# Performance work log

Measured on AMD Instinct MI355X. Metric: run time of the kernel, lower is better.

Reference implementation:

```python
import jax, jax.numpy as jnp
import numpy as np

N = 50000   # num nodes
R = 8       # num relations
E = 800000  # num edges
IN, HID, OUT = 128, 128, 64


def rgcn_layer(x, src, dst, etype, W, root, bias):
    """PyG-style RGCNConv: per-relation mean aggregation + root weight + bias.
    x: [N, I], W: [R, I, O], root: [I, O], bias: [O]."""
    O = W.shape[-1]
    # transform node features once per relation: [R, N, O]
    xr = jnp.einsum('ni,rio->rno', x, W)
    # per-edge message = relation-specific transform of source node
    m = xr[etype, src]                      # [E, O] gather
    # mean-aggregate per (relation, dst) pair, then sum over relations
    idx = etype * N + dst                   # combined segment id in [0, R*N)
    s = jax.ops.segment_sum(m, idx, num_segments=R * N)          # [R*N, O]
    c = jax.ops.segment_sum(jnp.ones_like(etype, dtype=m.dtype), idx,
                            num_segments=R * N)                   # [R*N]
    agg = (s / jnp.maximum(c, 1.0)[:, None]).reshape(R, N, O).sum(axis=0)
    return agg + x @ root + bias


def setup_inputs() -> dict:
    key = jax.random.key(0)
    ks = jax.random.split(key, 16)
    x = jax.random.normal(ks[0], (N, IN), dtype=jnp.float32)
    edge_index = jax.random.randint(ks[1], (2, E), 0, N, dtype=jnp.int32)
    edge_type = jax.random.randint(ks[2], (E,), 0, R, dtype=jnp.int32)
    dims = [(IN, HID), (HID, HID), (HID, HID), (HID, OUT)]
    inp = {"x": x, "edge_index": edge_index, "edge_type": edge_type}
    for li, (i, o) in enumerate(dims):
        sc = 1.0 / np.sqrt(i)
        inp[f"W{li+1}"] = jax.random.normal(ks[3 + 3 * li], (R, i, o), dtype=jnp.float32) * sc
        inp[f"root{li+1}"] = jax.random.normal(ks[4 + 3 * li], (i, o), dtype=jnp.float32) * sc
        inp[f"b{li+1}"] = jnp.zeros((o,), dtype=jnp.float32)
    return inp


def reference(x, edge_index, edge_type,
              W1, root1, b1, W2, root2, b2,
              W3, root3, b3, W4, root4, b4):
    src, dst = edge_index[0], edge_index[1]
    h = jax.nn.relu(rgcn_layer(x, src, dst, edge_type, W1, root1, b1))
    h = jax.nn.relu(rgcn_layer(h, src, dst, edge_type, W2, root2, b2))
    h = jax.nn.relu(rgcn_layer(h, src, dst, edge_type, W3, root3, b3))
    h = rgcn_layer(h, src, dst, edge_type, W4, root4, b4)
    return jax.nn.log_softmax(h, axis=1)
```

## Files before the change

kernel.cpp:

```cpp
#include <hip/hip_runtime.h>
#include <math.h>

#define NN 50000
#define RR 8
#define EE 800000
#define RN 400000
#define DIN 128
#define K1 1024
#define KTOT 1152
#define NBLK 391
#define LDWH 648

#define OFF_HB0  0UL
#define OFF_HB1  12800000UL
#define OFF_XB   25600000UL
#define OFF_LG   38400000UL
#define OFF_WT   51200000UL
#define OFF_OFFS 52379648UL
#define OFF_CUR  53979776UL
#define OFF_SRT  55579776UL
#define OFF_BS   58779776UL
#define WS_NEED  58783872UL

typedef short bf16x8 __attribute__((ext_vector_type(8)));
typedef float f32x4 __attribute__((ext_vector_type(4)));

__device__ __forceinline__ unsigned f2bf(float f) {
    unsigned x = __float_as_uint(f);
    return (x + 0x7fffu + ((x >> 16) & 1u)) >> 16;
}
__device__ __forceinline__ float bflo(unsigned p) { return __uint_as_float(p << 16); }
__device__ __forceinline__ float bfhi(unsigned p) { return __uint_as_float(p & 0xffff0000u); }

__global__ void k_cvt(const float* __restrict__ x, ushort* __restrict__ xb) {
    int i = blockIdx.x * 256 + threadIdx.x;
    if (i >= NN * 32) return;
    float4 v = ((const float4*)x)[i];
    ushort4 o;
    o.x = (ushort)f2bf(v.x); o.y = (ushort)f2bf(v.y);
    o.z = (ushort)f2bf(v.z); o.w = (ushort)f2bf(v.w);
    ((ushort4*)xb)[i] = o;
}

__global__ void k_wtall(const float* __restrict__ W0, const float* __restrict__ R0,
                        const float* __restrict__ W1, const float* __restrict__ R1,
                        const float* __restrict__ W2, const float* __restrict__ R2,
                        const float* __restrict__ W3, const float* __restrict__ R3,
                        ushort* __restrict__ WT) {
    int b = blockIdx.x;
    int layer = (b < 384) ? (b >> 7) : 3;
    int o = (b < 384) ? (b & 127) : (b - 384);
    int O = (layer == 3) ? 64 : 128;
    const float* W  = (layer == 0) ? W0 : (layer == 1) ? W1 : (layer == 2) ? W2 : W3;
    const float* Rt = (layer == 0) ? R0 : (layer == 1) ? R1 : (layer == 2) ? R2 : R3;
    ushort* dst = WT + (size_t)layer * 147456;
    for (int k = threadIdx.x; k < KTOT; k += 256) {
        float v = (k < K1)
            ? W[(size_t)(k >> 7) * 128 * O + (size_t)(k & 127) * O + o]
            : Rt[(size_t)(k - K1) * O + o];
        dst[(size_t)o * KTOT + k] = (ushort)f2bf(v);
    }
}

__global__ void k_hist(const int* __restrict__ ei, const int* __restrict__ et,
                       int* __restrict__ hist) {
    int e = blockIdx.x * blockDim.x + threadIdx.x;
    if (e >= EE) return;
    atomicAdd(&hist[ei[EE + e] * RR + et[e]], 1);
}

__global__ void k_scan1(const int* __restrict__ hist, int* __restrict__ offs,
                        int* __restrict__ bsums) {
    __shared__ int tmp[1024];
    int tid = threadIdx.x;
    int g = blockIdx.x * 1024 + tid;
    int v = (g < RN) ? hist[g] : 0;
    tmp[tid] = v;
    __syncthreads();
    for (int off = 1; off < 1024; off <<= 1) {
        int t = tmp[tid];
        if (tid >= off) t += tmp[tid - off];
        __syncthreads();
        tmp[tid] = t;
        __syncthreads();
    }
    if (g < RN) offs[g] = tmp[tid] - v;
    if (tid == 1023) bsums[blockIdx.x] = tmp[1023];
}

__global__ void k_scan2(int* __restrict__ bsums) {
    __shared__ int tmp[1024];
    int tid = threadIdx.x;
    int v = (tid < NBLK) ? bsums[tid] : 0;
    tmp[tid] = v;
    __syncthreads();
    for (int off = 1; off < 1024; off <<= 1) {
        int t = tmp[tid];
        if (tid >= off) t += tmp[tid - off];
        __syncthreads();
        tmp[tid] = t;
        __syncthreads();
    }
    if (tid < NBLK) bsums[tid] = tmp[tid] - v;
}

__global__ void k_scan3(int* __restrict__ offs, const int* __restrict__ bsums) {
    int g = blockIdx.x * 1024 + threadIdx.x;
    if (g < RN) offs[g] += bsums[blockIdx.x];
    else if (g == RN) offs[RN] = EE;
}

__global__ void k_scatter(const int* __restrict__ ei, const int* __restrict__ et,
                          const int* __restrict__ offs, int* __restrict__ cur,
                          int* __restrict__ ssrc) {
    int e = blockIdx.x * blockDim.x + threadIdx.x;
    if (e >= EE) return;
    int s = ei[EE + e] * RR + et[e];
    ssrc[offs[s] + atomicAdd(&cur[s], 1)] = ei[e];
}

template<int O, bool RELU, bool SMAX>
__global__ __launch_bounds__(512) void k_fused(
        const ushort* __restrict__ hb, const int* __restrict__ offs,
        const int* __restrict__ ssrc, const ushort* __restrict__ WT,
        const float* __restrict__ bias, void* __restrict__ outv) {
    __shared__ ushort As[32 * LDWH];
    const int tid = threadIdx.x;
    const int lane = tid & 63;
    const int w = tid >> 6;
    const int q = lane >> 4;
    const int ll = lane & 15;
    const int nbase = blockIdx.x * 32;
    const uint4* h16 = (const uint4*)hb;

    constexpr int NTILE = O / 16;
    const int cw = w % NTILE;
    const int mt0 = (NTILE == 8) ? 0 : (w / NTILE);
    constexpr int NMT = (NTILE == 8) ? 2 : 1;
    const int lr = lane & 15, hi = lane >> 4;
    f32x4 acc[NMT] = {};

    for (int half = 0; half < 2; ++half) {
        const int rbase = half * 4;
        for (int i = 0; i < 2; ++i) {
            int nlA = w * 4 + i * 2;
            int nlB = nlA + 1;
            int nA = min(nbase + nlA, NN - 1);
            int nB = min(nbase + nlB, NN - 1);
            int b = offs[((lane < 32) ? nA : nB) * 8 + rbase + min(lane & 31, 4)];
            int b0A = __shfl(b, 0),  b4A = __shfl(b, 4);
            int b0B = __shfl(b, 32), b4B = __shfl(b, 36);
            int nbA = b4A - b0A, nbB = b4B - b0B;
            int svA = ssrc[min(b0A + min(lane, max(nbA - 1, 0)), EE - 1)];
            int svB = ssrc[min(b0B + min(lane, max(nbB - 1, 0)), EE - 1)];
            int begA = __shfl(b, q),      endA = __shfl(b, q + 1);
            int begB = __shfl(b, 32 + q), endB = __shfl(b, 32 + q + 1);
            int lenA = endA - begA, lenB = endB - begB;
            int mxA = max(max(__shfl(lenA, 0), __shfl(lenA, 16)),
                          max(__shfl(lenA, 32), __shfl(lenA, 48)));
            int mxB = max(max(__shfl(lenB, 0), __shfl(lenB, 16)),
                          max(__shfl(lenB, 32), __shfl(lenB, 48)));
            int mx = max(mxA, mxB);
            int beglA = begA - b0A, beglB = begB - b0B;
            float aA0 = 0.f, aA1 = 0.f, aA2 = 0.f, aA3 = 0.f;
            float aA4 = 0.f, aA5 = 0.f, aA6 = 0.f, aA7 = 0.f;
            float aB0 = 0.f, aB1 = 0.f, aB2 = 0.f, aB3 = 0.f;
            float aB4 = 0.f, aB5 = 0.f, aB6 = 0.f, aB7 = 0.f;
            for (int j = 0; j < mx; j += 4) {
                int eA = beglA + j, eB = beglB + j;
                int sA0 = __shfl(svA, min(eA, 63));
                int sA1 = __shfl(svA, min(eA + 1, 63));
                int sA2 = __shfl(svA, min(eA + 2, 63));
                int sA3 = __shfl(svA, min(eA + 3, 63));
                int sB0 = __shfl(svB, min(eB, 63));
                int sB1 = __shfl(svB, min(eB + 1, 63));
                int sB2 = __shfl(svB, min(eB + 2, 63));
                int sB3 = __shfl(svB, min(eB + 3, 63));
                if (eA + 3 >= 64) {
                    sA0 = ssrc[min(b0A + eA, EE - 1)];
                    sA1 = ssrc[min(b0A + eA + 1, EE - 1)];
                    sA2 = ssrc[min(b0A + eA + 2, EE - 1)];
                    sA3 = ssrc[min(b0A + eA + 3, EE - 1)];
                }
                if (eB + 3 >= 64) {
                    sB0 = ssrc[min(b0B + eB, EE - 1)];
                    sB1 = ssrc[min(b0B + eB + 1, EE - 1)];
                    sB2 = ssrc[min(b0B + eB + 2, EE - 1)];
                    sB3 = ssrc[min(b0B + eB + 3, EE - 1)];
                }
                uint4 uA0 = h16[(size_t)sA0 * 16 + ll];
                uint4 uA1 = h16[(size_t)sA1 * 16 + ll];
                uint4 uA2 = h16[(size_t)sA2 * 16 + ll];
                uint4 uA3 = h16[(size_t)sA3 * 16 + ll];
                uint4 uB0 = h16[(size_t)sB0 * 16 + ll];
                uint4 uB1 = h16[(size_t)sB1 * 16 + ll];
                uint4 uB2 = h16[(size_t)sB2 * 16 + ll];
                uint4 uB3 = h16[(size_t)sB3 * 16 + ll];
                if (j < lenA) {
                    aA0 += bflo(uA0.x); aA1 += bfhi(uA0.x);
                    aA2 += bflo(uA0.y); aA3 += bfhi(uA0.y);
                    aA4 += bflo(uA0.z); aA5 += bfhi(uA0.z);
                    aA6 += bflo(uA0.w); aA7 += bfhi(uA0.w);
                }
                if (j + 1 < lenA) {
                    aA0 += bflo(uA1.x); aA1 += bfhi(uA1.x);
                    aA2 += bflo(uA1.y); aA3 += bfhi(uA1.y);
                    aA4 += bflo(uA1.z); aA5 += bfhi(uA1.z);
                    aA6 += bflo(uA1.w); aA7 += bfhi(uA1.w);
                }
                if (j + 2 < lenA) {
                    aA0 += bflo(uA2.x); aA1 += bfhi(uA2.x);
                    aA2 += bflo(uA2.y); aA3 += bfhi(uA2.y);
                    aA4 += bflo(uA2.z); aA5 += bfhi(uA2.z);
                    aA6 += bflo(uA2.w); aA7 += bfhi(uA2.w);
                }
                if (j + 3 < lenA) {
                    aA0 += bflo(uA3.x); aA1 += bfhi(uA3.x);
                    aA2 += bflo(uA3.y); aA3 += bfhi(uA3.y);
                    aA4 += bflo(uA3.z); aA5 += bfhi(uA3.z);
                    aA6 += bflo(uA3.w); aA7 += bfhi(uA3.w);
                }
                if (j < lenB) {
                    aB0 += bflo(uB0.x); aB1 += bfhi(uB0.x);
                    aB2 += bflo(uB0.y); aB3 += bfhi(uB0.y);
                    aB4 += bflo(uB0.z); aB5 += bfhi(uB0.z);
                    aB6 += bflo(uB0.w); aB7 += bfhi(uB0.w);
                }
                if (j + 1 < lenB) {
                    aB0 += bflo(uB1.x); aB1 += bfhi(uB1.x);
                    aB2 += bflo(uB1.y); aB3 += bfhi(uB1.y);
                    aB4 += bflo(uB1.z); aB5 += bfhi(uB1.z);
                    aB6 += bflo(uB1.w); aB7 += bfhi(uB1.w);
                }
                if (j + 2 < lenB) {
                    aB0 += bflo(uB2.x); aB1 += bfhi(uB2.x);
                    aB2 += bflo(uB2.y); aB3 += bfhi(uB2.y);
                    aB4 += bflo(uB2.z); aB5 += bfhi(uB2.z);
                    aB6 += bflo(uB2.w); aB7 += bfhi(uB2.w);
                }
                if (j + 3 < lenB) {
                    aB0 += bflo(uB3.x); aB1 += bfhi(uB3.x);
                    aB2 += bflo(uB3.y); aB3 += bfhi(uB3.y);
                    aB4 += bflo(uB3.z); aB5 += bfhi(uB3.z);
                    aB6 += bflo(uB3.w); aB7 += bfhi(uB3.w);
                }
            }
            float invA = 1.0f / (float)max(lenA, 1);
            float invB = 1.0f / (float)max(lenB, 1);
            uint4 oA, oB;
            oA.x = f2bf(aA0 * invA) | (f2bf(aA1 * invA) << 16);
            oA.y = f2bf(aA2 * invA) | (f2bf(aA3 * invA) << 16);
            oA.z = f2bf(aA4 * invA) | (f2bf(aA5 * invA) << 16);
            oA.w = f2bf(aA6 * invA) | (f2bf(aA7 * invA) << 16);
            oB.x = f2bf(aB0 * invB) | (f2bf(aB1 * invB) << 16);
            oB.y = f2bf(aB2 * invB) | (f2bf(aB3 * invB) << 16);
            oB.z = f2bf(aB4 * invB) | (f2bf(aB5 * invB) << 16);
            oB.w = f2bf(aB6 * invB) | (f2bf(aB7 * invB) << 16);
            *(uint4*)(&As[nlA * LDWH + (q * 16 + ll) * 8]) = oA;
            *(uint4*)(&As[nlB * LDWH + (q * 16 + ll) * 8]) = oB;
        }
        if (half == 1) {
            int row = tid >> 4;
            int cc = tid & 15;
            uint4 v = h16[(size_t)min(nbase + row, NN - 1) * 16 + cc];
            *(uint4*)(&As[row * LDWH + (64 + cc) * 8]) = v;
        }
        __syncthreads();
        const int KS = (half == 0) ? 16 : 20;
        const ushort* wcol = WT + (size_t)(cw * 16 + lr) * KTOT
                                + half * 512 + hi * 8;
        for (int ks = 0; ks < KS; ++ks) {
            bf16x8 bb = *(const bf16x8*)(wcol + ks * 32);
            int g = ks * 4 + hi;
#pragma unroll
            for (int m = 0; m < NMT; ++m) {
                int row = (mt0 + m) * 16 + lr;
                bf16x8 a = *(const bf16x8*)(&As[row * LDWH + g * 8]);
                acc[m] = __builtin_amdgcn_mfma_f32_16x16x32_bf16(a, bb, acc[m], 0, 0, 0);
            }
        }
        __syncthreads();
    }
    int col = cw * 16 + lr;
    float bs = bias[col];
    if (!SMAX) {
#pragma unroll
        for (int m = 0; m < NMT; ++m) {
#pragma unroll
            for (int j = 0; j < 4; ++j) {
                int row = nbase + (mt0 + m) * 16 + hi * 4 + j;
                if (row >= NN) continue;
                float v = acc[m][j] + bs;
                if (RELU) v = fmaxf(v, 0.f);
                ((ushort*)outv)[(size_t)row * O + col] = (ushort)f2bf(v);
            }
        }
    } else {
        float* Asf = (float*)As;
#pragma unroll
        for (int j = 0; j < 4; ++j) {
            int rl = mt0 * 16 + hi * 4 + j;
            Asf[rl * 65 + col] = acc[0][j] + bs;
        }
        __syncthreads();
        for (int rr = 0; rr < 4; ++rr) {
            int rl = w * 4 + rr;
            float v = Asf[rl * 65 + lane];
            float m = v;
#pragma unroll
            for (int off = 32; off; off >>= 1) m = fmaxf(m, __shfl_xor(m, off, 64));
            float e = expf(v - m);
            float s = e;
#pragma unroll
            for (int off = 32; off; off >>= 1) s += __shfl_xor(s, off, 64);
            int row = nbase + rl;
            if (row < NN)
                ((float*)outv)[(size_t)row * 64 + lane] = v - m - logf(s);
        }
    }
}

extern "C" void kernel_launch(void* const* d_in, const int* in_sizes, int n_in,
                              void* d_out, int out_size, void* d_ws, size_t ws_size,
                              hipStream_t stream) {
    const float* x  = (const float*)d_in[0];
    const int*   ei = (const int*)d_in[1];
    const int*   et = (const int*)d_in[2];
    const float* W[4]    = {(const float*)d_in[3], (const float*)d_in[6],
                            (const float*)d_in[9], (const float*)d_in[12]};
    const float* root[4] = {(const float*)d_in[4], (const float*)d_in[7],
                            (const float*)d_in[10], (const float*)d_in[13]};
    const float* bias[4] = {(const float*)d_in[5], (const float*)d_in[8],
                            (const float*)d_in[11], (const float*)d_in[14]};

    if (ws_size < WS_NEED) return;

    char* ws = (char*)d_ws;
    ushort* hb0  = (ushort*)(ws + OFF_HB0);
    ushort* hb1  = (ushort*)(ws + OFF_HB1);
    ushort* xb   = (ushort*)(ws + OFF_XB);
    ushort* WT   = (ushort*)(ws + OFF_WT);
    int*   offs  = (int*)(ws + OFF_OFFS);
    int*   cur   = (int*)(ws + OFF_CUR);
    int*   ssrc  = (int*)(ws + OFF_SRT);
    int*   bsums = (int*)(ws + OFF_BS);
    ushort* WTl[4] = {WT, WT + 147456, WT + 2 * 147456, WT + 3 * 147456};

    k_cvt<<<(NN * 32 + 255) / 256, 256, 0, stream>>>(x, xb);
    k_wtall<<<448, 256, 0, stream>>>(W[0], root[0], W[1], root[1],
                                     W[2], root[2], W[3], root[3], WT);

    hipMemsetAsync(cur, 0, RN * sizeof(int), stream);
    k_hist<<<(EE + 255) / 256, 256, 0, stream>>>(ei, et, cur);
    k_scan1<<<NBLK, 1024, 0, stream>>>(cur, offs, bsums);
    k_scan2<<<1, 1024, 0, stream>>>(bsums);
    k_scan3<<<NBLK + 1, 1024, 0, stream>>>(offs, bsums);
    hipMemsetAsync(cur, 0, RN * sizeof(int), stream);
    k_scatter<<<(EE + 255) / 256, 256, 0, stream>>>(ei, et, offs, cur, ssrc);

    const int G = (NN + 31) / 32;
    k_fused<128, true,  false><<<G, 512, 0, stream>>>(xb,  offs, ssrc, WTl[0], bias[0], hb0);
    k_fused<128, true,  false><<<G, 512, 0, stream>>>(hb0, offs, ssrc, WTl[1], bias[1], hb1);
    k_fused<128, true,  false><<<G, 512, 0, stream>>>(hb1, offs, ssrc, WTl[2], bias[2], hb0);
    k_fused<64,  false, true ><<<G, 512, 0, stream>>>(hb0, offs, ssrc, WTl[3], bias[3], d_out);
}
```

Before: 515.8 us.

## Aggregate all eight relations before a single full-K MFMA pass

The fused gather+GEMM kernel used to run two halves, each aggregating four relations into shared memory and then running a partial MFMA pass. It now aggregates all eight relations first, writing one row of 1152 bf16 values per node into a larger shared tile, and then runs one fully unrolled 36-step MFMA loop. The aim is to cut barrier count and loop overhead and to load the neighbour-offset row and edge list once per node pair instead of once per half. In exchange the shared tile roughly doubles (about 74KB), which may reduce how many blocks fit per CU, and the edge gather and GEMM phases no longer interleave across halves.

```diff
diff --git a/kernel.cpp b/kernel.cpp
--- a/kernel.cpp
+++ b/kernel.cpp
@@ -9,12 +9,11 @@
 #define K1 1024
 #define KTOT 1152
 #define NBLK 391
-#define LDWH 648
+#define LDW 1160
 
 #define OFF_HB0  0UL
 #define OFF_HB1  12800000UL
 #define OFF_XB   25600000UL
-#define OFF_LG   38400000UL
 #define OFF_WT   51200000UL
 #define OFF_OFFS 52379648UL
 #define OFF_CUR  53979776UL
@@ -124,7 +123,7 @@
         const ushort* __restrict__ hb, const int* __restrict__ offs,
         const int* __restrict__ ssrc, const ushort* __restrict__ WT,
         const float* __restrict__ bias, void* __restrict__ outv) {
-    __shared__ ushort As[32 * LDWH];
+    __shared__ ushort As[32 * LDW];
     const int tid = threadIdx.x;
     const int lane = tid & 63;
     const int w = tid >> 6;
@@ -133,28 +132,22 @@
     const int nbase = blockIdx.x * 32;
     const uint4* h16 = (const uint4*)hb;
 
-    constexpr int NTILE = O / 16;
-    const int cw = w % NTILE;
-    const int mt0 = (NTILE == 8) ? 0 : (w / NTILE);
-    constexpr int NMT = (NTILE == 8) ? 2 : 1;
-    const int lr = lane & 15, hi = lane >> 4;
-    f32x4 acc[NMT] = {};
-
-    for (int half = 0; half < 2; ++half) {
-        const int rbase = half * 4;
-        for (int i = 0; i < 2; ++i) {
-            int nlA = w * 4 + i * 2;
-            int nlB = nlA + 1;
-            int nA = min(nbase + nlA, NN - 1);
-            int nB = min(nbase + nlB, NN - 1);
-            int b = offs[((lane < 32) ? nA : nB) * 8 + rbase + min(lane & 31, 4)];
-            int b0A = __shfl(b, 0),  b4A = __shfl(b, 4);
-            int b0B = __shfl(b, 32), b4B = __shfl(b, 36);
-            int nbA = b4A - b0A, nbB = b4B - b0B;
-            int svA = ssrc[min(b0A + min(lane, max(nbA - 1, 0)), EE - 1)];
-            int svB = ssrc[min(b0B + min(lane, max(nbB - 1, 0)), EE - 1)];
-            int begA = __shfl(b, q),      endA = __shfl(b, q + 1);
-            int begB = __shfl(b, 32 + q), endB = __shfl(b, 32 + q + 1);
+    for (int i = 0; i < 2; ++i) {
+        int nlA = w * 4 + i * 2;
+        int nlB = nlA + 1;
+        int nA = min(nbase + nlA, NN - 1);
+        int nB = min(nbase + nlB, NN - 1);
+        int b = offs[((lane < 32) ? nA : nB) * 8 + min(lane & 31, 8)];
+        int b0A = __shfl(b, 0),  b8A = __shfl(b, 8);
+        int b0B = __shfl(b, 32), b8B = __shfl(b, 40);
+        int nbA = b8A - b0A, nbB = b8B - b0B;
+        int svA = ssrc[min(b0A + min(lane, max(nbA - 1, 0)), EE - 1)];
+        int svB = ssrc[min(b0B + min(lane, max(nbB - 1, 0)), EE - 1)];
+#pragma unroll
+        for (int p = 0; p < 2; ++p) {
+            int r = p * 4 + q;
+            int begA = __shfl(b, r),      endA = __shfl(b, r + 1);
+            int begB = __shfl(b, 32 + r), endB = __shfl(b, 32 + r + 1);
             int lenA = endA - begA, lenB = endB - begB;
             int mxA = max(max(__shfl(lenA, 0), __shfl(lenA, 16)),
                           max(__shfl(lenA, 32), __shfl(lenA, 48)));
@@ -256,30 +249,34 @@
             oB.y = f2bf(aB2 * invB) | (f2bf(aB3 * invB) << 16);
             oB.z = f2bf(aB4 * invB) | (f2bf(aB5 * invB) << 16);
             oB.w = f2bf(aB6 * invB) | (f2bf(aB7 * invB) << 16);
-            *(uint4*)(&As[nlA * LDWH + (q * 16 + ll) * 8]) = oA;
-            *(uint4*)(&As[nlB * LDWH + (q * 16 + ll) * 8]) = oB;
-        }
-        if (half == 1) {
-            int row = tid >> 4;
-            int cc = tid & 15;
-            uint4 v = h16[(size_t)min(nbase + row, NN - 1) * 16 + cc];
-            *(uint4*)(&As[row * LDWH + (64 + cc) * 8]) = v;
-        }
-        __syncthreads();
-        const int KS = (half == 0) ? 16 : 20;
-        const ushort* wcol = WT + (size_t)(cw * 16 + lr) * KTOT
-                                + half * 512 + hi * 8;
-        for (int ks = 0; ks < KS; ++ks) {
-            bf16x8 bb = *(const bf16x8*)(wcol + ks * 32);
-            int g = ks * 4 + hi;
-#pragma unroll
-            for (int m = 0; m < NMT; ++m) {
-                int row = (mt0 + m) * 16 + lr;
-                bf16x8 a = *(const bf16x8*)(&As[row * LDWH + g * 8]);
-                acc[m] = __builtin_amdgcn_mfma_f32_16x16x32_bf16(a, bb, acc[m], 0, 0, 0);
-            }
-        }
-        __syncthreads();
+            *(uint4*)(&As[nlA * LDW + (r * 16 + ll) * 8]) = oA;
+            *(uint4*)(&As[nlB * LDW + (r * 16 + ll) * 8]) = oB;
+        }
+    }
+    {
+        int row = tid >> 4;
+        int cc = tid & 15;
+        uint4 v = h16[(size_t)min(nbase + row, NN - 1) * 16 + cc];
+        *(uint4*)(&As[row * LDW + (128 + cc) * 8]) = v;
+    }
+    __syncthreads();
+    constexpr int NTILE = O / 16;
+    const int cw = w % NTILE;
+    const int mt0 = (NTILE == 8) ? 0 : (w / NTILE);
+    constexpr int NMT = (NTILE == 8) ? 2 : 1;
+    const int lr = lane & 15, hi = lane >> 4;
+    f32x4 acc[NMT] = {};
+    const ushort* wcol = WT + (size_t)(cw * 16 + lr) * KTOT + hi * 8;
+#pragma unroll
+    for (int ks = 0; ks < 36; ++ks) {
+        bf16x8 bb = *(const bf16x8*)(wcol + ks * 32);
+        int g = ks * 4 + hi;
+#pragma unroll
+        for (int m = 0; m < NMT; ++m) {
+            int row = (mt0 + m) * 16 + lr;
+            bf16x8 a = *(const bf16x8*)(&As[row * LDW + g * 8]);
+            acc[m] = __builtin_amdgcn_mfma_f32_16x16x32_bf16(a, bb, acc[m], 0, 0, 0);
+        }
     }
     int col = cw * 16 + lr;
     float bs = bias[col];
@@ -296,6 +293,7 @@
             }
         }
     } else {
+        __syncthreads();
         float* Asf = (float*)As;
 #pragma unroll
         for (int j = 0; j < 4; ++j) {
```

After: 507.6 us. About the same (-1.6%).
